# Optimization experiments

Hardware: AMD Instinct MI355X
Metric: run time of the kernel (lower is better)

## Reference

```python
import jax, jax.numpy as jnp
import numpy as np
from jax import lax

NUM_BINS = 8


def setup_inputs() -> dict:
    key = jax.random.key(0)
    kx, kc, kw = jax.random.split(key, 3)
    N, H, W, C = 8, 128, 128, 64
    x = jax.random.uniform(kx, (N, H, W, C), dtype=jnp.float32)
    # he_normal-style initializers for the learned tables
    co_matrix = jax.random.normal(kc, (NUM_BINS, NUM_BINS), dtype=jnp.float32) * np.sqrt(2.0 / NUM_BINS)
    w_spatial = jax.random.normal(kw, (3, 3), dtype=jnp.float32) * np.sqrt(2.0 / 9.0)
    return {"x": x, "co_matrix": co_matrix, "w_spatial": w_spatial}


def reference(x, co_matrix, w_spatial):
    """Co-occurrence layer: y(p) = sum_b co[bin(x_p), b] * conv(x * 1[bin(x)==b], w)(p).

    This is the vectorized form of the per-bin tf.while_loop in CoLL.call:
    quantize input into num_bins buckets, run the spatial filter on each
    bin-masked copy of x, then gather the co-occurrence row for each output
    element's bin and accumulate across bins.
    """
    num_bins = co_matrix.shape[0]
    N, H, W, C = x.shape
    k = w_spatial.shape[0]

    # --- quantization_input_as_bins: uniform bins over [min, max] ---
    xmin = jnp.min(x)
    xmax = jnp.max(x)
    scale = num_bins / (xmax - xmin + jnp.asarray(1e-8, x.dtype))
    idx = jnp.clip(jnp.floor((x - xmin) * scale), 0, num_bins - 1).astype(jnp.int32)  # [N,H,W,C]

    # --- per-bin masked copies of x: [N,H,W,C,B] -> fold into channels ---
    onehot = jax.nn.one_hot(idx, num_bins, dtype=x.dtype)           # [N,H,W,C,B]
    xb = (x[..., None] * onehot).reshape(N, H, W, C * num_bins)     # [N,H,W,C*B]

    # --- shared spatial filter applied depthwise to every (channel, bin) slice ---
    kern = jnp.broadcast_to(w_spatial[:, :, None, None], (k, k, 1, C * num_bins))  # HWIO depthwise
    z = lax.conv_general_dilated(
        xb, kern,
        window_strides=(1, 1), padding="SAME",
        dimension_numbers=("NHWC", "HWIO", "NHWC"),
        feature_group_count=C * num_bins,
    ).reshape(N, H, W, C, num_bins)                                  # [N,H,W,C,B]

    # --- gather co-occurrence row by the output element's bin, accumulate ---
    co_rows = co_matrix[idx]                                         # [N,H,W,C,B]
    y = jnp.sum(co_rows * z, axis=-1)                                # [N,H,W,C]
    return y
```

## Files before the change

### kernel.cpp

```cpp
#include <hip/hip_runtime.h>


static constexpr int IMG4 = 128 * 128 * 16;
static constexpr int TOT4 = 8 * IMG4;
static constexpr int RBLK = 2048;
static constexpr int RSTRIDE = RBLK * 256;
static constexpr int NBLK = 1024, NTHR = 256;

__device__ __forceinline__ int qbin(float v, float xmin, float scale) {
    float t = (v - xmin) * scale;
    t = fminf(t, 7.0f);
    return (int)t;
}

__global__ __launch_bounds__(256) void reduce_k(const float4* __restrict__ x4,
                                                float2* __restrict__ part) {
    const int i = blockIdx.x * 256 + threadIdx.x;
    float4 a = x4[i];
    float4 b = x4[i + RSTRIDE];
    float4 c = x4[i + 2 * RSTRIDE];
    float4 d = x4[i + 3 * RSTRIDE];
    float lmin = fminf(fminf(fminf(a.x, a.y), fminf(a.z, a.w)),
                       fminf(fminf(b.x, b.y), fminf(b.z, b.w)));
    float lmax = fmaxf(fmaxf(fmaxf(a.x, a.y), fmaxf(a.z, a.w)),
                       fmaxf(fmaxf(b.x, b.y), fmaxf(b.z, b.w)));
    lmin = fminf(lmin, fminf(fminf(fminf(c.x, c.y), fminf(c.z, c.w)),
                             fminf(fminf(d.x, d.y), fminf(d.z, d.w))));
    lmax = fmaxf(lmax, fmaxf(fmaxf(fmaxf(c.x, c.y), fmaxf(c.z, c.w)),
                             fmaxf(fmaxf(d.x, d.y), fmaxf(d.z, d.w))));
#pragma unroll
    for (int off = 32; off; off >>= 1) {
        lmin = fminf(lmin, __shfl_xor(lmin, off, 64));
        lmax = fmaxf(lmax, __shfl_xor(lmax, off, 64));
    }
    __shared__ float smin[4], smax[4];
    const int wid = threadIdx.x >> 6, lane = threadIdx.x & 63;
    if (lane == 0) { smin[wid] = lmin; smax[wid] = lmax; }
    __syncthreads();
    if (threadIdx.x == 0) {
        part[blockIdx.x] = make_float2(
            fminf(fminf(smin[0], smin[1]), fminf(smin[2], smin[3])),
            fmaxf(fmaxf(smax[0], smax[1]), fmaxf(smax[2], smax[3])));
    }
}

__global__ __launch_bounds__(256) void coll_k(const float4* __restrict__ x4,
                                              const float* __restrict__ co,
                                              const float* __restrict__ wsp,
                                              float4* __restrict__ y4,
                                              const float2* __restrict__ part) {
    __shared__ float sred[8];

    float gmin = 3.4028235e38f, gmax = -3.4028235e38f;
#pragma unroll
    for (int j = 0; j < 8; ++j) {
        float2 p = part[threadIdx.x * 8 + j];
        gmin = fminf(gmin, p.x);
        gmax = fmaxf(gmax, p.y);
    }
#pragma unroll
    for (int off = 32; off; off >>= 1) {
        gmin = fminf(gmin, __shfl_xor(gmin, off, 64));
        gmax = fmaxf(gmax, __shfl_xor(gmax, off, 64));
    }
    const int wid = threadIdx.x >> 6, lane = threadIdx.x & 63;
    if (lane == 0) { sred[wid] = gmin; sred[4 + wid] = gmax; }
    __syncthreads();
    const float xmin = fminf(fminf(sred[0], sred[1]), fminf(sred[2], sred[3]));
    const float xmax = fmaxf(fmaxf(sred[4], sred[5]), fmaxf(sred[6], sred[7]));
    const float scale = 8.0f / ((xmax - xmin) + 1e-8f);

    const int co_i = __float_as_int(co[lane]);

    const int ofs = blockIdx.x * 256 + threadIdx.x;
    const int w = (ofs >> 4) & 127;
    const int h = (ofs >> 11) & 127;
    const bool wm = (w > 0), wp = (w < 127), hm = (h > 0), hp = (h < 127);

    const bool v0 = hm && wm, v1 = hm, v2 = hm && wp;
    const bool v3 = wm,                v5 = wp;
    const bool v6 = hp && wm, v7 = hp, v8 = hp && wp;

    const float wz0 = v0 ? wsp[0] : 0.f, wz1 = v1 ? wsp[1] : 0.f;
    const float wz2 = v2 ? wsp[2] : 0.f, wz3 = v3 ? wsp[3] : 0.f;
    const float wz4 = wsp[4];
    const float wz5 = v5 ? wsp[5] : 0.f, wz6 = v6 ? wsp[6] : 0.f;
    const float wz7 = v7 ? wsp[7] : 0.f, wz8 = v8 ? wsp[8] : 0.f;

#pragma unroll 1
    for (int k = 0; k < 8; ++k) {
        const int base = k * IMG4 + ofs;

        const float4 qc = x4[base];
        const float4 q0 = x4[v0 ? base - 2064 : base];
        const float4 q1 = x4[v1 ? base - 2048 : base];
        const float4 q2 = x4[v2 ? base - 2032 : base];
        const float4 q3 = x4[v3 ? base - 16   : base];
        const float4 q5 = x4[v5 ? base + 16   : base];
        const float4 q6 = x4[v6 ? base + 2032 : base];
        const float4 q7 = x4[v7 ? base + 2048 : base];
        const float4 q8 = x4[v8 ? base + 2064 : base];

        const int ip4x = qbin(qc.x, xmin, scale) << 5;
        const int ip4y = qbin(qc.y, xmin, scale) << 5;
        const int ip4z = qbin(qc.z, xmin, scale) << 5;
        const int ip4w = qbin(qc.w, xmin, scale) << 5;

        float ax = 0.f, ay = 0.f, az = 0.f, aw = 0.f;

#define ACC(Q, WZ) { \
        const int a_x = ip4x + (qbin(Q.x, xmin, scale) << 2); \
        const int a_y = ip4y + (qbin(Q.y, xmin, scale) << 2); \
        const int a_z = ip4z + (qbin(Q.z, xmin, scale) << 2); \
        const int a_w = ip4w + (qbin(Q.w, xmin, scale) << 2); \
        ax = fmaf((WZ) * Q.x, __int_as_float(__builtin_amdgcn_ds_bpermute(a_x, co_i)), ax); \
        ay = fmaf((WZ) * Q.y, __int_as_float(__builtin_amdgcn_ds_bpermute(a_y, co_i)), ay); \
        az = fmaf((WZ) * Q.z, __int_as_float(__builtin_amdgcn_ds_bpermute(a_z, co_i)), az); \
        aw = fmaf((WZ) * Q.w, __int_as_float(__builtin_amdgcn_ds_bpermute(a_w, co_i)), aw); }

        ACC(q0, wz0) ACC(q1, wz1) ACC(q2, wz2)
        ACC(q3, wz3) ACC(qc, wz4) ACC(q5, wz5)
        ACC(q6, wz6) ACC(q7, wz7) ACC(q8, wz8)
#undef ACC

        y4[base] = make_float4(ax, ay, az, aw);
    }
}

extern "C" void kernel_launch(void* const* d_in, const int* in_sizes, int n_in,
                              void* d_out, int out_size, void* d_ws, size_t ws_size,
                              hipStream_t stream) {
    const float4* x4 = (const float4*)d_in[0];
    const float*  co = (const float*)d_in[1];
    const float*  wsp = (const float*)d_in[2];
    float4* y4 = (float4*)d_out;
    float2* part = (float2*)d_ws;

    hipLaunchKernelGGL(reduce_k, dim3(RBLK), dim3(NTHR), 0, stream, x4, part);
    hipLaunchKernelGGL(coll_k, dim3(NBLK), dim3(NTHR), 0, stream,
                       x4, co, wsp, y4, part);
}
```

Baseline: 103.4 us.

## Compute two output rows per thread to reuse shared neighbor loads and bins

Each thread now produces outputs for two vertically adjacent rows (h0 and h0+1). It loads a 4x3 neighborhood once and quantizes each neighbor once, sharing both across the two outputs, and the grid is halved to match. This cuts redundant global loads and qbin work per output. In exchange each thread holds more registers and the grid has half as many threads, which may lower occupancy and latency hiding.

Result: slower. 109.0 us (+5.5%).

```diff
diff --git a/kernel.cpp b/kernel.cpp
--- a/kernel.cpp
+++ b/kernel.cpp
@@ -5,7 +5,7 @@
 static constexpr int TOT4 = 8 * IMG4;
 static constexpr int RBLK = 2048;
 static constexpr int RSTRIDE = RBLK * 256;
-static constexpr int NBLK = 1024, NTHR = 256;
+static constexpr int CBLK = 512, NTHR = 256;
 
 __device__ __forceinline__ int qbin(float v, float xmin, float scale) {
     float t = (v - xmin) * scale;
@@ -72,59 +72,89 @@
 
     const int co_i = __float_as_int(co[lane]);
 
-    const int ofs = blockIdx.x * 256 + threadIdx.x;
-    const int w = (ofs >> 4) & 127;
-    const int h = (ofs >> 11) & 127;
-    const bool wm = (w > 0), wp = (w < 127), hm = (h > 0), hp = (h < 127);
+    const int i = blockIdx.x * 256 + threadIdx.x;
+    const int c4 = i & 15;
+    const int w  = (i >> 4) & 127;
+    const int hb = i >> 11;
+    const int h0 = hb << 1;
 
-    const bool v0 = hm && wm, v1 = hm, v2 = hm && wp;
-    const bool v3 = wm,                v5 = wp;
-    const bool v6 = hp && wm, v7 = hp, v8 = hp && wp;
+    const bool vm = (w > 0), vp = (w < 127);
+    const bool vt = (h0 > 0), vb = (hb < 63);
 
-    const float wz0 = v0 ? wsp[0] : 0.f, wz1 = v1 ? wsp[1] : 0.f;
-    const float wz2 = v2 ? wsp[2] : 0.f, wz3 = v3 ? wsp[3] : 0.f;
-    const float wz4 = wsp[4];
-    const float wz5 = v5 ? wsp[5] : 0.f, wz6 = v6 ? wsp[6] : 0.f;
-    const float wz7 = v7 ? wsp[7] : 0.f, wz8 = v8 ? wsp[8] : 0.f;
+    const int o4 = h0 * 2048 + w * 16 + c4;
+    const int o0 = (vt && vm) ? o4 - 2064 : o4, o1 = vt ? o4 - 2048 : o4;
+    const int o2 = (vt && vp) ? o4 - 2032 : o4, o3 = vm ? o4 - 16 : o4;
+    const int o5 = vp ? o4 + 16 : o4,           o6 = vm ? o4 + 2032 : o4;
+    const int o7 = o4 + 2048;
+    const int o8 = vp ? o4 + 2064 : o4;
+    const int o9 = (vb && vm) ? o4 + 4080 : o4, o10 = vb ? o4 + 4096 : o4;
+    const int o11 = (vb && vp) ? o4 + 4112 : o4;
+
+    const float s0 = wsp[0], s1 = wsp[1], s2 = wsp[2], s3 = wsp[3], s4 = wsp[4],
+                s5 = wsp[5], s6 = wsp[6], s7 = wsp[7], s8 = wsp[8];
+    const float z00 = (vt && vm) ? s0 : 0.f, z01 = vt ? s1 : 0.f,
+                z02 = (vt && vp) ? s2 : 0.f;
+    const float z03 = vm ? s3 : 0.f, z04 = s4, z05 = vp ? s5 : 0.f;
+    const float z06 = vm ? s6 : 0.f, z07 = s7, z08 = vp ? s8 : 0.f;
+    const float z10 = vm ? s0 : 0.f, z11 = s1, z12 = vp ? s2 : 0.f;
+    const float z13 = vm ? s3 : 0.f, z14 = s4, z15 = vp ? s5 : 0.f;
+    const float z16 = (vb && vm) ? s6 : 0.f, z17 = vb ? s7 : 0.f,
+                z18 = (vb && vp) ? s8 : 0.f;
+
+#define BP(A) __int_as_float(__builtin_amdgcn_ds_bpermute((A), co_i))
 
 #pragma unroll 1
     for (int k = 0; k < 8; ++k) {
-        const int base = k * IMG4 + ofs;
+        const int kb = k * IMG4;
+        const float4 q0 = x4[kb + o0], q1 = x4[kb + o1], q2 = x4[kb + o2];
+        const float4 q3 = x4[kb + o3], q4 = x4[kb + o4], q5 = x4[kb + o5];
+        const float4 q6 = x4[kb + o6], q7 = x4[kb + o7], q8 = x4[kb + o8];
+        const float4 q9 = x4[kb + o9], q10 = x4[kb + o10], q11 = x4[kb + o11];
 
-        const float4 qc = x4[base];
-        const float4 q0 = x4[v0 ? base - 2064 : base];
-        const float4 q1 = x4[v1 ? base - 2048 : base];
-        const float4 q2 = x4[v2 ? base - 2032 : base];
-        const float4 q3 = x4[v3 ? base - 16   : base];
-        const float4 q5 = x4[v5 ? base + 16   : base];
-        const float4 q6 = x4[v6 ? base + 2032 : base];
-        const float4 q7 = x4[v7 ? base + 2048 : base];
-        const float4 q8 = x4[v8 ? base + 2064 : base];
+        const int i0x = qbin(q4.x, xmin, scale) << 5;
+        const int i0y = qbin(q4.y, xmin, scale) << 5;
+        const int i0z = qbin(q4.z, xmin, scale) << 5;
+        const int i0w = qbin(q4.w, xmin, scale) << 5;
+        const int i1x = qbin(q7.x, xmin, scale) << 5;
+        const int i1y = qbin(q7.y, xmin, scale) << 5;
+        const int i1z = qbin(q7.z, xmin, scale) << 5;
+        const int i1w = qbin(q7.w, xmin, scale) << 5;
 
-        const int ip4x = qbin(qc.x, xmin, scale) << 5;
-        const int ip4y = qbin(qc.y, xmin, scale) << 5;
-        const int ip4z = qbin(qc.z, xmin, scale) << 5;
-        const int ip4w = qbin(qc.w, xmin, scale) << 5;
+        float a0x = 0.f, a0y = 0.f, a0z = 0.f, a0w = 0.f;
+        float a1x = 0.f, a1y = 0.f, a1z = 0.f, a1w = 0.f;
+        int bx, by, bz, bw;
 
-        float ax = 0.f, ay = 0.f, az = 0.f, aw = 0.f;
+#define QB4(Q) { bx = qbin(Q.x, xmin, scale) << 2; by = qbin(Q.y, xmin, scale) << 2; \
+                 bz = qbin(Q.z, xmin, scale) << 2; bw = qbin(Q.w, xmin, scale) << 2; }
+#define ACC0(Q, WZ) { a0x = fmaf((WZ) * Q.x, BP(i0x + bx), a0x); \
+                      a0y = fmaf((WZ) * Q.y, BP(i0y + by), a0y); \
+                      a0z = fmaf((WZ) * Q.z, BP(i0z + bz), a0z); \
+                      a0w = fmaf((WZ) * Q.w, BP(i0w + bw), a0w); }
+#define ACC1(Q, WZ) { a1x = fmaf((WZ) * Q.x, BP(i1x + bx), a1x); \
+                      a1y = fmaf((WZ) * Q.y, BP(i1y + by), a1y); \
+                      a1z = fmaf((WZ) * Q.z, BP(i1z + bz), a1z); \
+                      a1w = fmaf((WZ) * Q.w, BP(i1w + bw), a1w); }
 
-#define ACC(Q, WZ) { \
-        const int a_x = ip4x + (qbin(Q.x, xmin, scale) << 2); \
-        const int a_y = ip4y + (qbin(Q.y, xmin, scale) << 2); \
-        const int a_z = ip4z + (qbin(Q.z, xmin, scale) << 2); \
-        const int a_w = ip4w + (qbin(Q.w, xmin, scale) << 2); \
-        ax = fmaf((WZ) * Q.x, __int_as_float(__builtin_amdgcn_ds_bpermute(a_x, co_i)), ax); \
-        ay = fmaf((WZ) * Q.y, __int_as_float(__builtin_amdgcn_ds_bpermute(a_y, co_i)), ay); \
-        az = fmaf((WZ) * Q.z, __int_as_float(__builtin_amdgcn_ds_bpermute(a_z, co_i)), az); \
-        aw = fmaf((WZ) * Q.w, __int_as_float(__builtin_amdgcn_ds_bpermute(a_w, co_i)), aw); }
+        QB4(q0)  ACC0(q0, z00)
+        QB4(q1)  ACC0(q1, z01)
+        QB4(q2)  ACC0(q2, z02)
+        QB4(q3)  ACC0(q3, z03)  ACC1(q3, z10)
+        QB4(q4)  ACC0(q4, z04)  ACC1(q4, z11)
+        QB4(q5)  ACC0(q5, z05)  ACC1(q5, z12)
+        QB4(q6)  ACC0(q6, z06)  ACC1(q6, z13)
+        QB4(q7)  ACC0(q7, z07)  ACC1(q7, z14)
+        QB4(q8)  ACC0(q8, z08)  ACC1(q8, z15)
+        QB4(q9)  ACC1(q9, z16)
+        QB4(q10) ACC1(q10, z17)
+        QB4(q11) ACC1(q11, z18)
+#undef QB4
+#undef ACC0
+#undef ACC1
 
-        ACC(q0, wz0) ACC(q1, wz1) ACC(q2, wz2)
-        ACC(q3, wz3) ACC(qc, wz4) ACC(q5, wz5)
-        ACC(q6, wz6) ACC(q7, wz7) ACC(q8, wz8)
-#undef ACC
-
-        y4[base] = make_float4(ax, ay, az, aw);
+        y4[kb + o4] = make_float4(a0x, a0y, a0z, a0w);
+        y4[kb + o7] = make_float4(a1x, a1y, a1z, a1w);
     }
+#undef BP
 }
 
 extern "C" void kernel_launch(void* const* d_in, const int* in_sizes, int n_in,
@@ -137,6 +167,6 @@
     float2* part = (float2*)d_ws;
 
     hipLaunchKernelGGL(reduce_k, dim3(RBLK), dim3(NTHR), 0, stream, x4, part);
-    hipLaunchKernelGGL(coll_k, dim3(NBLK), dim3(NTHR), 0, stream,
+    hipLaunchKernelGGL(coll_k, dim3(CBLK), dim3(NTHR), 0, stream,
                        x4, co, wsp, y4, part);
 }
```
